# Optimization experiments

Measured on AMD Instinct MI355X. Metric: run time of the kernel, lower is better.

The kernel has to match this reference:

```python
import jax, jax.numpy as jnp
import numpy as np

K = 64  # init kwarg k
B, D = 4096, 16384


def setup_inputs() -> dict:
    key = jax.random.key(0)
    x = jax.random.normal(key, (B, D), dtype=jnp.float32)
    return {"x": x}


def reference(x):
    # top-k along last dim, then scatter values into a zero tensor (same as
    # torch.topk + zeros_like + scatter_).
    vals, idx = jax.lax.top_k(x, K)            # [B, K], [B, K]
    rows = jnp.arange(x.shape[0])[:, None]     # [B, 1] broadcast against idx
    return jnp.zeros_like(x).at[rows, idx].set(vals)
```

## Files before the change

kernel.cpp:

```cpp
#include <hip/hip_runtime.h>


#define TK_D      16384
#define TK_K      64
#define TK_BLOCK  512
#define TK_NF4    8
#define TK_VPT    32
#define TK_EQCAP  1024

__launch_bounds__(TK_BLOCK, 4)
__global__ void topk_scatter_kernel(const float* __restrict__ x,
                                    float* __restrict__ out) {
    __shared__ int      sh_hist[256];
    __shared__ unsigned sh_prefix;
    __shared__ int      sh_rem;
    __shared__ unsigned sh_counts;
    __shared__ int      sh_eqn;
    __shared__ int      sh_eqidx[TK_EQCAP];

    const int row = blockIdx.x;
    const int tid = threadIdx.x;
    const float4* __restrict__ xrow = (const float4*)(x + (size_t)row * TK_D);
    float4* __restrict__ orow       = (float4*)(out + (size_t)row * TK_D);

    unsigned u[TK_VPT];
    #pragma unroll
    for (int k = 0; k < TK_NF4; k++) {
        float4 v = xrow[tid + k * TK_BLOCK];
        unsigned b0 = __float_as_uint(v.x);
        unsigned b1 = __float_as_uint(v.y);
        unsigned b2 = __float_as_uint(v.z);
        unsigned b3 = __float_as_uint(v.w);
        u[4*k+0] = b0 ^ ((unsigned)((int)b0 >> 31) | 0x80000000u);
        u[4*k+1] = b1 ^ ((unsigned)((int)b1 >> 31) | 0x80000000u);
        u[4*k+2] = b2 ^ ((unsigned)((int)b2 >> 31) | 0x80000000u);
        u[4*k+3] = b3 ^ ((unsigned)((int)b3 >> 31) | 0x80000000u);
    }

    if (tid == 0) { sh_prefix = 0u; sh_rem = TK_K; sh_counts = 0u; sh_eqn = 0; }

    #pragma unroll
    for (int p = 0; p < 4; p++) {
        if (tid < 256) sh_hist[tid] = 0;
        __syncthreads();
        const unsigned pref = sh_prefix;
        const int      rem  = sh_rem;
        const int      shift = 24 - 8 * p;
        #pragma unroll
        for (int i = 0; i < TK_VPT; i++) {
            bool in_scope = (p == 0) || ((u[i] >> (shift + 8)) == pref);
            if (in_scope) atomicAdd(&sh_hist[(u[i] >> shift) & 0xFF], 1);
        }
        __syncthreads();
        if (tid < 64) {
            const int lane = tid;
            int h0 = sh_hist[4*lane+0], h1 = sh_hist[4*lane+1];
            int h2 = sh_hist[4*lane+2], h3 = sh_hist[4*lane+3];
            int local = h0 + h1 + h2 + h3;
            int suf = local;
            #pragma unroll
            for (int off = 1; off < 64; off <<= 1) {
                int o = __shfl_down(suf, off);
                if (lane + off < 64) suf += o;
            }
            int A  = suf - local;
            int S3 = A + h3, S2 = S3 + h2, S1 = S2 + h1, S0 = S1 + h0;
            int d = -1, ab = 0;
            if      (S3 >= rem && A  < rem) { d = 4*lane+3; ab = A;  }
            else if (S2 >= rem && S3 < rem) { d = 4*lane+2; ab = S3; }
            else if (S1 >= rem && S2 < rem) { d = 4*lane+1; ab = S2; }
            else if (S0 >= rem && S1 < rem) { d = 4*lane+0; ab = S1; }
            if (d >= 0) {
                sh_prefix = (pref << 8) | (unsigned)d;
                sh_rem    = rem - ab;
            }
        }
        __syncthreads();
    }
    const unsigned T = sh_prefix;

    {
        int cgt = 0, ceq = 0;
        #pragma unroll
        for (int i = 0; i < TK_VPT; i++) { cgt += (u[i] > T); ceq += (u[i] == T); }
        unsigned packed = (unsigned)cgt | ((unsigned)ceq << 16);
        #pragma unroll
        for (int off = 32; off > 0; off >>= 1)
            packed += __shfl_down(packed, off);
        if ((tid & 63) == 0) atomicAdd(&sh_counts, packed);
    }

    const float Tf = __uint_as_float(T ^ ((unsigned)((int)(~T) >> 31) | 0x80000000u));

    #pragma unroll
    for (int k = 0; k < TK_NF4; k++) {
        float4 o;
        const int base = 4 * (tid + k * TK_BLOCK);
        #pragma unroll
        for (int c = 0; c < 4; c++) {
            unsigned uu = u[4*k+c];
            float f = __uint_as_float(uu ^ ((unsigned)((int)(~uu) >> 31) | 0x80000000u));
            ((float*)&o)[c] = (uu > T) ? f : 0.0f;
            if (uu == T) {
                int pos = atomicAdd(&sh_eqn, 1);
                if (pos < TK_EQCAP) sh_eqidx[pos] = base + c;
            }
        }
        orow[tid + k * TK_BLOCK] = o;
    }
    __syncthreads();

    const unsigned cnts = sh_counts;
    const int c_gt = (int)(cnts & 0xFFFFu);
    const int need = TK_K - c_gt;
    const int L = min(sh_eqn, TK_EQCAP);
    for (int i = tid; i < L; i += TK_BLOCK) {
        int col  = sh_eqidx[i];
        int rank = 0;
        for (int j = 0; j < L; j++) rank += (sh_eqidx[j] < col);
        if (rank < need) out[(size_t)row * TK_D + col] = Tf;
    }
}

extern "C" void kernel_launch(void* const* d_in, const int* in_sizes, int n_in,
                              void* d_out, int out_size, void* d_ws, size_t ws_size,
                              hipStream_t stream) {
    const float* x = (const float*)d_in[0];
    float* out = (float*)d_out;
    const int B = in_sizes[0] / TK_D;
    topk_scatter_kernel<<<B, TK_BLOCK, 0, stream>>>(x, out);
}
```

Before: 466.2 us.

## Stage row in LDS via global_load_lds and use 3-pass 11-bit radix select

Each row is now loaded straight into shared memory with the async global-to-LDS load builtin instead of being held in 32 registers per thread. The radix select now uses three passes of 11/11/10 bits with a 2048-bin histogram in place of four 8-bit passes. The histogram scan is spread across all eight wavefronts, and the tie count comes from the remaining rank rather than an extra counting pass. The aim is fewer passes and syncs and lower register pressure. In exchange each block uses about 64KB of LDS, which limits how many blocks fit on a CU, and every pass rereads the values from LDS.

```diff
diff --git a/kernel.cpp b/kernel.cpp
--- a/kernel.cpp
+++ b/kernel.cpp
@@ -5,120 +5,129 @@
 #define TK_K      64
 #define TK_BLOCK  512
 #define TK_NF4    8
-#define TK_VPT    32
+#define TK_BINS   2048
 #define TK_EQCAP  1024
+
+__device__ __forceinline__ unsigned ord_map(unsigned b) {
+    return b ^ ((unsigned)((int)b >> 31) | 0x80000000u);
+}
 
 __launch_bounds__(TK_BLOCK, 4)
 __global__ void topk_scatter_kernel(const float* __restrict__ x,
                                     float* __restrict__ out) {
-    __shared__ int      sh_hist[256];
+    __shared__ __align__(16) unsigned sh_vals[TK_D];
+    __shared__ int      sh_hist[TK_BINS];
+    __shared__ int      sh_wsum[8];
     __shared__ unsigned sh_prefix;
     __shared__ int      sh_rem;
-    __shared__ unsigned sh_counts;
     __shared__ int      sh_eqn;
     __shared__ int      sh_eqidx[TK_EQCAP];
 
-    const int row = blockIdx.x;
-    const int tid = threadIdx.x;
+    const int row  = blockIdx.x;
+    const int tid  = threadIdx.x;
+    const int lane = tid & 63;
+    const int wv   = tid >> 6;
+
     const float4* __restrict__ xrow = (const float4*)(x + (size_t)row * TK_D);
-    float4* __restrict__ orow       = (float4*)(out + (size_t)row * TK_D);
 
-    unsigned u[TK_VPT];
     #pragma unroll
-    for (int k = 0; k < TK_NF4; k++) {
-        float4 v = xrow[tid + k * TK_BLOCK];
-        unsigned b0 = __float_as_uint(v.x);
-        unsigned b1 = __float_as_uint(v.y);
-        unsigned b2 = __float_as_uint(v.z);
-        unsigned b3 = __float_as_uint(v.w);
-        u[4*k+0] = b0 ^ ((unsigned)((int)b0 >> 31) | 0x80000000u);
-        u[4*k+1] = b1 ^ ((unsigned)((int)b1 >> 31) | 0x80000000u);
-        u[4*k+2] = b2 ^ ((unsigned)((int)b2 >> 31) | 0x80000000u);
-        u[4*k+3] = b3 ^ ((unsigned)((int)b3 >> 31) | 0x80000000u);
+    for (int i = 0; i < TK_NF4; i++) {
+        const int c4 = wv * 64 + i * TK_BLOCK;
+        __builtin_amdgcn_global_load_lds(
+            (const __attribute__((address_space(1))) void*)(xrow + c4 + lane),
+            (__attribute__((address_space(3))) void*)(&sh_vals[4 * c4]),
+            16, 0, 0);
     }
 
-    if (tid == 0) { sh_prefix = 0u; sh_rem = TK_K; sh_counts = 0u; sh_eqn = 0; }
+    ((int4*)sh_hist)[tid] = int4{0, 0, 0, 0};
+    if (tid == 0) { sh_prefix = 0u; sh_rem = TK_K; sh_eqn = 0; }
+    __syncthreads();
 
-    #pragma unroll
-    for (int p = 0; p < 4; p++) {
-        if (tid < 256) sh_hist[tid] = 0;
-        __syncthreads();
+    const int histshift[3]  = {21, 10, 0};
+    const int scopeshift[3] = {0, 21, 10};
+    const int nbits[3]      = {11, 11, 10};
+
+    for (int p = 0; p < 3; p++) {
         const unsigned pref = sh_prefix;
         const int      rem  = sh_rem;
-        const int      shift = 24 - 8 * p;
+        const int      hs   = histshift[p];
+        const unsigned msk  = (1u << nbits[p]) - 1u;
         #pragma unroll
-        for (int i = 0; i < TK_VPT; i++) {
-            bool in_scope = (p == 0) || ((u[i] >> (shift + 8)) == pref);
-            if (in_scope) atomicAdd(&sh_hist[(u[i] >> shift) & 0xFF], 1);
-        }
-        __syncthreads();
-        if (tid < 64) {
-            const int lane = tid;
-            int h0 = sh_hist[4*lane+0], h1 = sh_hist[4*lane+1];
-            int h2 = sh_hist[4*lane+2], h3 = sh_hist[4*lane+3];
-            int local = h0 + h1 + h2 + h3;
-            int suf = local;
+        for (int i = 0; i < TK_NF4; i++) {
+            uint4 b = ((const uint4*)sh_vals)[tid + i * TK_BLOCK];
             #pragma unroll
-            for (int off = 1; off < 64; off <<= 1) {
-                int o = __shfl_down(suf, off);
-                if (lane + off < 64) suf += o;
-            }
-            int A  = suf - local;
-            int S3 = A + h3, S2 = S3 + h2, S1 = S2 + h1, S0 = S1 + h0;
-            int d = -1, ab = 0;
-            if      (S3 >= rem && A  < rem) { d = 4*lane+3; ab = A;  }
-            else if (S2 >= rem && S3 < rem) { d = 4*lane+2; ab = S3; }
-            else if (S1 >= rem && S2 < rem) { d = 4*lane+1; ab = S2; }
-            else if (S0 >= rem && S1 < rem) { d = 4*lane+0; ab = S1; }
-            if (d >= 0) {
-                sh_prefix = (pref << 8) | (unsigned)d;
-                sh_rem    = rem - ab;
+            for (int c = 0; c < 4; c++) {
+                unsigned u = ord_map(((const unsigned*)&b)[c]);
+                bool in_scope = (p == 0) || ((u >> scopeshift[p] >> nbits[0]) == pref);
+                in_scope = (p == 0) || ((u >> (hs + nbits[p])) == pref);
+                if (in_scope) atomicAdd(&sh_hist[(u >> hs) & msk], 1);
             }
         }
         __syncthreads();
-    }
-    const unsigned T = sh_prefix;
 
-    {
-        int cgt = 0, ceq = 0;
+        int h0 = sh_hist[4 * tid + 0], h1 = sh_hist[4 * tid + 1];
+        int h2 = sh_hist[4 * tid + 2], h3 = sh_hist[4 * tid + 3];
+        int local = h0 + h1 + h2 + h3;
+        int suf = local;
         #pragma unroll
-        for (int i = 0; i < TK_VPT; i++) { cgt += (u[i] > T); ceq += (u[i] == T); }
-        unsigned packed = (unsigned)cgt | ((unsigned)ceq << 16);
+        for (int off = 1; off < 64; off <<= 1) {
+            int o = __shfl_down(suf, off);
+            if (lane + off < 64) suf += o;
+        }
+        if (lane == 0) sh_wsum[wv] = suf;
+        __syncthreads();
+
+        ((int4*)sh_hist)[tid] = int4{0, 0, 0, 0};
+
+        int above = 0;
         #pragma unroll
-        for (int off = 32; off > 0; off >>= 1)
-            packed += __shfl_down(packed, off);
-        if ((tid & 63) == 0) atomicAdd(&sh_counts, packed);
+        for (int w2 = 0; w2 < 8; w2++)
+            if (w2 > wv) above += sh_wsum[w2];
+
+        int a3 = above + (suf - local);
+        int S3 = a3 + h3, S2 = S3 + h2, S1 = S2 + h1, S0 = S1 + h0;
+        int d = -1, ab = 0;
+        if      (S3 >= rem && a3 < rem) { d = 4 * tid + 3; ab = a3; }
+        else if (S2 >= rem && S3 < rem) { d = 4 * tid + 2; ab = S3; }
+        else if (S1 >= rem && S2 < rem) { d = 4 * tid + 1; ab = S2; }
+        else if (S0 >= rem && S1 < rem) { d = 4 * tid + 0; ab = S1; }
+        if (d >= 0) {
+            sh_prefix = (pref << nbits[p]) | (unsigned)d;
+            sh_rem    = rem - ab;
+        }
+        __syncthreads();
     }
 
-    const float Tf = __uint_as_float(T ^ ((unsigned)((int)(~T) >> 31) | 0x80000000u));
+    const unsigned T    = sh_prefix;
+    const int      need = sh_rem;
 
+    float4* __restrict__ orow = (float4*)(out + (size_t)row * TK_D);
     #pragma unroll
-    for (int k = 0; k < TK_NF4; k++) {
+    for (int i = 0; i < TK_NF4; i++) {
+        const int c4 = tid + i * TK_BLOCK;
+        uint4 b = ((const uint4*)sh_vals)[c4];
         float4 o;
-        const int base = 4 * (tid + k * TK_BLOCK);
         #pragma unroll
         for (int c = 0; c < 4; c++) {
-            unsigned uu = u[4*k+c];
-            float f = __uint_as_float(uu ^ ((unsigned)((int)(~uu) >> 31) | 0x80000000u));
-            ((float*)&o)[c] = (uu > T) ? f : 0.0f;
-            if (uu == T) {
+            unsigned raw = ((const unsigned*)&b)[c];
+            unsigned u   = ord_map(raw);
+            ((float*)&o)[c] = (u > T) ? __uint_as_float(raw) : 0.0f;
+            if (u == T) {
                 int pos = atomicAdd(&sh_eqn, 1);
-                if (pos < TK_EQCAP) sh_eqidx[pos] = base + c;
+                if (pos < TK_EQCAP) sh_eqidx[pos] = 4 * c4 + c;
             }
         }
-        orow[tid + k * TK_BLOCK] = o;
+        orow[c4] = o;
     }
     __syncthreads();
 
-    const unsigned cnts = sh_counts;
-    const int c_gt = (int)(cnts & 0xFFFFu);
-    const int need = TK_K - c_gt;
     const int L = min(sh_eqn, TK_EQCAP);
     for (int i = tid; i < L; i += TK_BLOCK) {
         int col  = sh_eqidx[i];
         int rank = 0;
         for (int j = 0; j < L; j++) rank += (sh_eqidx[j] < col);
-        if (rank < need) out[(size_t)row * TK_D + col] = Tf;
+        if (rank < need)
+            out[(size_t)row * TK_D + col] = __uint_as_float(sh_vals[col]);
     }
 }
 
```

Result: faster. 444.6 us (-4.6%).
